# Kernel tuning notes

Hardware: AMD Instinct MI355X
Metric: run time of the kernel (lower is better)

Reference implementation:

```python
import jax, jax.numpy as jnp
import numpy as np

NUM_HEADS = 16
BN_EPS = 1e-5


def setup_inputs() -> dict:
    key = jax.random.key(0)
    ks = jax.random.split(key, 12)
    B, S, D = 8, 1024, 1024
    s = 1.0 / np.sqrt(D)
    return {
        "key": jax.random.normal(ks[0], (B, S, D), jnp.float32),
        "value": jax.random.normal(ks[1], (B, S, D), jnp.float32),
        "query": jax.random.normal(ks[2], (B, S, D), jnp.float32),
        "Wk": jax.random.normal(ks[3], (D, D), jnp.float32) * s,
        "bk": jax.random.normal(ks[4], (D,), jnp.float32) * s,
        "Wv": jax.random.normal(ks[5], (D, D), jnp.float32) * s,
        "bv": jax.random.normal(ks[6], (D,), jnp.float32) * s,
        "Wq": jax.random.normal(ks[7], (D, D), jnp.float32) * s,
        "bq": jax.random.normal(ks[8], (D,), jnp.float32) * s,
        "Wf": jax.random.normal(ks[9], (D, D), jnp.float32) * s,
        "bf": jax.random.normal(ks[10], (D,), jnp.float32) * s,
        "gamma": jnp.ones((D,), jnp.float32),
        "beta": jnp.zeros((D,), jnp.float32),
    }


def _mha(key, value, query, Wk, bk, Wv, bv, Wq, bq, Wf, bf, gamma, beta):
    B, S, D = query.shape
    H = NUM_HEADS
    d = D // H
    residual = query

    k = key @ Wk + bk      # [B, S, D]
    v = value @ Wv + bv
    q = query @ Wq + bq

    # Faithful to torch: raw row-major view(B*H, -1, d) — NOT the standard head transpose.
    k = k.reshape(B * H, -1, d)   # [B*H, S, d]
    v = v.reshape(B * H, -1, d)
    q = q.reshape(B * H, -1, d)

    # Faithful quirky scale: (dim_per_head // num_heads) ** -0.5
    scale = jnp.float32((d // H) ** (-0.5))

    scores = jnp.einsum('bqd,bkd->bqk', q, k) * scale          # [B*H, S, S]
    attention = jax.nn.softmax(scores, axis=2)
    context = jnp.einsum('bqk,bkd->bqd', attention, v)          # [B*H, S, d]

    context = context.reshape(B, -1, D)                         # [B, S, D]
    out = context @ Wf + bf

    # BatchNorm1d over channel dim D (training mode: batch stats over B and S, biased var)
    x = residual + out                                          # [B, S, D]
    mean = jnp.mean(x, axis=(0, 1))
    var = jnp.mean((x - mean) ** 2, axis=(0, 1))
    out = (x - mean) * jax.lax.rsqrt(var + BN_EPS) * gamma + beta
    return out, attention


def reference(key, value, query, Wk, bk, Wv, bv, Wq, bq, Wf, bf, gamma, beta):
    return _mha(key, value, query, Wk, bk, Wv, bv, Wq, bq, Wf, bf, gamma, beta)
```

## Files before the change

### kernel.cpp

```cpp
#include <hip/hip_runtime.h>
#include <hip/hip_bf16.h>
#include <stdint.h>

typedef __attribute__((ext_vector_type(8))) short     short8;
typedef __attribute__((ext_vector_type(8))) _Float16  f16x8;
typedef __attribute__((ext_vector_type(4))) float     f32x4;
typedef __attribute__((ext_vector_type(4))) unsigned short ushort4_t;

__device__ inline unsigned short f2bf(float f) {
    unsigned u = __float_as_uint(f);
    u += 0x7fffu + ((u >> 16) & 1u);
    return (unsigned short)(u >> 16);
}
__device__ inline float bf2f(unsigned short h) {
    return __uint_as_float(((unsigned)h) << 16);
}
__device__ inline unsigned short f2h(float f) {
    _Float16 h = (_Float16)f;
    unsigned short r;
    __builtin_memcpy(&r, &h, 2);
    return r;
}

__device__ inline void gload16(const void* g, void* lds) {
    unsigned loff = (unsigned)(uintptr_t)lds;
    loff = __builtin_amdgcn_readfirstlane(loff);
    auto l = (__attribute__((address_space(3))) unsigned int*)(uintptr_t)loff;
    auto p = (const __attribute__((address_space(1))) unsigned int*)(uintptr_t)g;
    __builtin_amdgcn_global_load_lds(p, l, 16, 0, 0);
}

__global__ void cvt3_f32_2b(const float4* __restrict__ k, const float4* __restrict__ q,
                            const float4* __restrict__ v,
                            ushort4_t* __restrict__ k16, ushort4_t* __restrict__ q16,
                            ushort4_t* __restrict__ v16, int n4) {
    const int which = blockIdx.y;
    const float4* in  = which == 0 ? k   : which == 1 ? q   : v;
    ushort4_t*    out = which == 0 ? k16 : which == 1 ? q16 : v16;
    const bool tof16 = (which < 2);
    for (int i = blockIdx.x * blockDim.x + threadIdx.x; i < n4; i += gridDim.x * blockDim.x) {
        float4 vv = in[i];
        ushort4_t r;
        if (tof16) { r.x = f2h(vv.x);  r.y = f2h(vv.y);  r.z = f2h(vv.z);  r.w = f2h(vv.w); }
        else       { r.x = f2bf(vv.x); r.y = f2bf(vv.y); r.z = f2bf(vv.z); r.w = f2bf(vv.w); }
        out[i] = r;
    }
}

__global__ void transpose_cvt4(const float* __restrict__ Wk, const float* __restrict__ Wq,
                               const float* __restrict__ Wv, const float* __restrict__ Wf,
                               unsigned short* __restrict__ WkT, unsigned short* __restrict__ WqT,
                               unsigned short* __restrict__ WvT, unsigned short* __restrict__ WfT) {
    const int which = blockIdx.z;
    const float* W = which == 0 ? Wk : which == 1 ? Wq : which == 2 ? Wv : Wf;
    unsigned short* WT = which == 0 ? WkT : which == 1 ? WqT : which == 2 ? WvT : WfT;
    const bool tof16 = (which < 2);
    const int dim = 1024;

    __shared__ float t[32][33];
    const int bx = blockIdx.x * 32, by = blockIdx.y * 32;
    const int tx = threadIdx.x, ty = threadIdx.y;
#pragma unroll
    for (int i = 0; i < 4; ++i)
        t[ty + 8 * i][tx] = W[(size_t)(by + ty + 8 * i) * dim + bx + tx];
    __syncthreads();
#pragma unroll
    for (int i = 0; i < 4; ++i) {
        float v = t[tx][ty + 8 * i];
        WT[(size_t)(bx + ty + 8 * i) * dim + by + tx] = tof16 ? f2h(v) : f2bf(v);
    }
}

__global__ void transpose_v(const unsigned short* __restrict__ v, unsigned short* __restrict__ vT) {
    const int bh = blockIdx.z, d0 = blockIdx.x * 32, s0 = blockIdx.y * 32;
    __shared__ unsigned short t[32][33];
    const int tx = threadIdx.x, ty = threadIdx.y;
    const size_t base = (size_t)bh << 16;
#pragma unroll
    for (int i = 0; i < 4; ++i)
        t[ty + 8 * i][tx] = v[base + (size_t)(s0 + ty + 8 * i) * 64 + d0 + tx];
    __syncthreads();
#pragma unroll
    for (int i = 0; i < 4; ++i)
        vT[base + (size_t)(d0 + ty + 8 * i) * 1024 + s0 + tx] = t[tx][ty + 8 * i];
}

template<int F16IN, int EPI>
__global__ __launch_bounds__(256, 2) void gemm_bt(
    const unsigned short* __restrict__ A,
    const unsigned short* __restrict__ Bt,
    const float* __restrict__ bias,
    unsigned short* __restrict__ C2b,
    const float* __restrict__ resid,
    float* __restrict__ Cf,
    int M, int N, int K, int nbx)
{
    const int bid = blockIdx.x;
    const int cpx = gridDim.x >> 3;
    const int swz = (bid & 7) * cpx + (bid >> 3);
    const int bm = swz / nbx, bn = swz % nbx;
    const int m0 = bm * 128, n0 = bn * 128;

    const int tid = threadIdx.x;
    const int w = tid >> 6, l = tid & 63, g = l >> 4, c = l & 15;
    const int wr = w >> 1, wc = w & 1;

    __shared__ unsigned short As[2][8192];
    __shared__ unsigned short Bs[2][8192];

    f32x4 acc[4][4] = {};

    const int srow = tid >> 3, scol = (tid & 7) * 8;
    const unsigned short* ApS = A  + (size_t)(m0 + srow) * K + scol;
    const unsigned short* BpS = Bt + (size_t)(n0 + srow) * K + scol;

    const int NT = K >> 6;

#define STAGE_GEMM(bufi, koff)                                                \
    do {                                                                      \
        _Pragma("unroll")                                                     \
        for (int i = 0; i < 4; ++i) {                                         \
            gload16(ApS + (size_t)i * 32 * K + (koff), &As[bufi][(i * 256 + tid - l) * 8]); \
            gload16(BpS + (size_t)i * 32 * K + (koff), &Bs[bufi][(i * 256 + tid - l) * 8]); \
        }                                                                     \
    } while (0)

#define COMPUTE_GEMM(bufi)                                                         \
    do {                                                                           \
        _Pragma("unroll")                                                          \
        for (int kk = 0; kk < 2; ++kk) {                                           \
            if constexpr (F16IN) {                                                 \
                f16x8 a[4], b[4];                                                  \
                _Pragma("unroll")                                                  \
                for (int mt = 0; mt < 4; ++mt)                                     \
                    a[mt] = *(const f16x8*)&As[bufi][(wr * 64 + mt * 16 + c) * 64 + kk * 32 + g * 8]; \
                _Pragma("unroll")                                                  \
                for (int nt = 0; nt < 4; ++nt)                                     \
                    b[nt] = *(const f16x8*)&Bs[bufi][(wc * 64 + nt * 16 + c) * 64 + kk * 32 + g * 8]; \
                _Pragma("unroll")                                                  \
                for (int mt = 0; mt < 4; ++mt)                                     \
                    _Pragma("unroll")                                              \
                    for (int nt = 0; nt < 4; ++nt)                                 \
                        acc[mt][nt] = __builtin_amdgcn_mfma_f32_16x16x32_f16(a[mt], b[nt], acc[mt][nt], 0, 0, 0); \
            } else {                                                               \
                short8 a[4], b[4];                                                 \
                _Pragma("unroll")                                                  \
                for (int mt = 0; mt < 4; ++mt)                                     \
                    a[mt] = *(const short8*)&As[bufi][(wr * 64 + mt * 16 + c) * 64 + kk * 32 + g * 8]; \
                _Pragma("unroll")                                                  \
                for (int nt = 0; nt < 4; ++nt)                                     \
                    b[nt] = *(const short8*)&Bs[bufi][(wc * 64 + nt * 16 + c) * 64 + kk * 32 + g * 8]; \
                _Pragma("unroll")                                                  \
                for (int mt = 0; mt < 4; ++mt)                                     \
                    _Pragma("unroll")                                              \
                    for (int nt = 0; nt < 4; ++nt)                                 \
                        acc[mt][nt] = __builtin_amdgcn_mfma_f32_16x16x32_bf16(a[mt], b[nt], acc[mt][nt], 0, 0, 0); \
            }                                                                      \
        }                                                                          \
    } while (0)

    STAGE_GEMM(0, 0);

#pragma unroll 2
    for (int kt = 0; kt < NT - 1; ++kt) {
        const int cur = kt & 1;
        STAGE_GEMM(cur ^ 1, (kt + 1) * 64);
        asm volatile("s_waitcnt vmcnt(8)" ::: "memory");
        __builtin_amdgcn_s_barrier();
        __builtin_amdgcn_sched_barrier(0);
        COMPUTE_GEMM(cur);
        __builtin_amdgcn_sched_barrier(0);
        __builtin_amdgcn_s_barrier();
    }
    asm volatile("s_waitcnt vmcnt(0)" ::: "memory");
    __builtin_amdgcn_s_barrier();
    __builtin_amdgcn_sched_barrier(0);
    COMPUTE_GEMM((NT - 1) & 1);

#undef STAGE_GEMM
#undef COMPUTE_GEMM

#pragma unroll
    for (int nt = 0; nt < 4; ++nt) {
        const int col = n0 + wc * 64 + nt * 16 + c;
        const float bs = bias[col];
#pragma unroll
        for (int mt = 0; mt < 4; ++mt) {
            const int row0 = m0 + wr * 64 + mt * 16 + g * 4;
#pragma unroll
            for (int r = 0; r < 4; ++r) {
                const float x = acc[mt][nt][r] + bs;
                const size_t idx = (size_t)(row0 + r) * N + col;
                if constexpr (EPI == 0) {
                    C2b[idx] = F16IN ? f2h(x) : f2bf(x);
                } else {
                    Cf[idx] = x + resid[idx];
                }
            }
        }
    }
}

__global__ __launch_bounds__(256, 4) void attn_kernel(
    const unsigned short* __restrict__ qf,
    const unsigned short* __restrict__ kf,
    const unsigned short* __restrict__ vT,
    float* __restrict__ attn_out,
    unsigned short* __restrict__ ctx)
{
    const int L = blockIdx.x;
    const int rb = (L >> 3) & 63;
    const int bh = ((L & 7) << 4) | (L >> 9);

    const int tid = threadIdx.x;
    const int w = tid >> 6, l = tid & 63, g = l >> 4, c = l & 15;
    const int n0 = w * 256;

    __shared__ unsigned short P[16 * 1024];
    __shared__ float rs_lds[4][16];
    __shared__ float inv_lds[16];

    const unsigned short* qb = qf + ((size_t)bh << 16) + (size_t)(rb * 16 + c) * 64 + g * 8;
    const f16x8 q0 = *(const f16x8*)(qb);
    const f16x8 q1 = *(const f16x8*)(qb + 32);

    const unsigned short* kb = kf + ((size_t)bh << 16);
    const unsigned swzc = ((unsigned)(c & 7)) << 4;
    const unsigned prow = (unsigned)c * 2048;

    ushort4_t pks[16];
    float rsum = 0.f;

#pragma unroll
    for (int t = 0; t < 16; ++t) {
        const unsigned short* kp = kb + (size_t)(n0 + t * 16 + c) * 64 + g * 8;
        const f16x8 a0 = *(const f16x8*)(kp);
        const f16x8 a1 = *(const f16x8*)(kp + 32);
        f32x4 s = {0.f, 0.f, 0.f, 0.f};
        s = __builtin_amdgcn_mfma_f32_16x16x32_f16(a0, q0, s, 0, 0, 0);
        s = __builtin_amdgcn_mfma_f32_16x16x32_f16(a1, q1, s, 0, 0, 0);

        const float p0 = __expf(s[0] * 0.5f);
        const float p1 = __expf(s[1] * 0.5f);
        const float p2 = __expf(s[2] * 0.5f);
        const float p3 = __expf(s[3] * 0.5f);
        rsum += (p0 + p1) + (p2 + p3);

        ushort4_t pk;
        pk.x = f2bf(p0); pk.y = f2bf(p1); pk.z = f2bf(p2); pk.w = f2bf(p3);
        pks[t] = pk;
        *(ushort4_t*)((char*)P + ((prow + (unsigned)(n0 * 2 + t * 32 + g * 8)) ^ swzc)) = pk;
    }

    rsum += __shfl_xor(rsum, 16);
    rsum += __shfl_xor(rsum, 32);
    if (g == 0) rs_lds[w][c] = rsum;
    __syncthreads();
    if (tid < 16)
        inv_lds[tid] = 1.0f / (rs_lds[0][tid] + rs_lds[1][tid] + rs_lds[2][tid] + rs_lds[3][tid]);
    __syncthreads();

    const int rA = l >> 3, jj = l & 7;
    const int rB = 8 + rA;
    const int slA = ((jj & 3) << 4) | rA;
    const int slB = ((jj & 3) << 4) | rB;
    const float invA = inv_lds[rA];
    const float invB = inv_lds[rB];
    float* aoA = attn_out + ((size_t)bh << 20) + (size_t)(rb * 16 + rA) * 1024 + n0;
    float* aoB = attn_out + ((size_t)bh << 20) + (size_t)(rb * 16 + rB) * 1024 + n0;

    f32x4 pacc = {0.f, 0.f, 0.f, 0.f};
    const unsigned short* vb = vT + ((size_t)bh << 16) + (size_t)(w * 16 + c) * 1024;
#pragma unroll
    for (int ks = 0; ks < 32; ++ks) {
        const short8 a = *(const short8*)((char*)P + ((prow + (unsigned)(ks * 64 + g * 16)) ^ swzc));
        const short8 b = *(const short8*)(vb + ks * 32 + g * 8);
        pacc = __builtin_amdgcn_mfma_f32_16x16x32_bf16(a, b, pacc, 0, 0, 0);
        if (ks & 1) {
            const int p = ks >> 2;
            const int t0 = 2 * p, t1 = t0 + 1;
            const bool isA = ((ks & 3) == 1);
            const int sl = isA ? slA : slB;
            unsigned long long e0, e1;
            __builtin_memcpy(&e0, &pks[t0], 8);
            __builtin_memcpy(&e1, &pks[t1], 8);
            const unsigned long long ea = __shfl(e0, sl, 64);
            const unsigned long long eb = __shfl(e1, sl, 64);
            const unsigned long long sel = (jj < 4) ? ea : eb;
            const float inv2 = isA ? invA : invB;
            f32x4 o;
            o[0] = bf2f((unsigned short)(sel      )) * inv2;
            o[1] = bf2f((unsigned short)(sel >> 16)) * inv2;
            o[2] = bf2f((unsigned short)(sel >> 32)) * inv2;
            o[3] = bf2f((unsigned short)(sel >> 48)) * inv2;
            float* dst = (isA ? aoA : aoB) + p * 32 + jj * 4;
            __builtin_nontemporal_store(o, (f32x4*)dst);
        }
    }
    unsigned short* cb = ctx + ((size_t)bh << 16) + (size_t)(rb * 16) * 64 + w * 16 + c;
#pragma unroll
    for (int r = 0; r < 4; ++r) {
        const int row = g * 4 + r;
        cb[(size_t)row * 64] = f2bf(pacc[r] * inv_lds[row]);
    }
}

__global__ void bn_stats(const float* __restrict__ x, float* __restrict__ psum, float* __restrict__ psq) {
    const int col = blockIdx.y * 256 + threadIdx.x;
    const int r0 = blockIdx.x * 128;
    float s = 0.f, q = 0.f;
#pragma unroll 4
    for (int r = 0; r < 128; ++r) {
        const float v = x[(size_t)(r0 + r) * 1024 + col];
        s += v; q += v * v;
    }
    psum[blockIdx.x * 1024 + col] = s;
    psq [blockIdx.x * 1024 + col] = q;
}

__global__ void bn_final(const float* __restrict__ psum, const float* __restrict__ psq,
                         const float* __restrict__ gamma, const float* __restrict__ beta,
                         float* __restrict__ ab) {
    const int cidx = threadIdx.x;
    float s = 0.f, q = 0.f;
#pragma unroll 8
    for (int i = 0; i < 64; ++i) { s += psum[i * 1024 + cidx]; q += psq[i * 1024 + cidx]; }
    const float mean = s * (1.0f / 8192.0f);
    const float var  = q * (1.0f / 8192.0f) - mean * mean;
    const float a = gamma[cidx] * rsqrtf(var + 1e-5f);
    ab[cidx]        = a;
    ab[1024 + cidx] = beta[cidx] - mean * a;
}

__global__ void bn_apply(const float4* __restrict__ x4, const float* __restrict__ ab, float4* __restrict__ o4) {
    const int n4 = 2 * 1024 * 1024;
    for (int i = blockIdx.x * blockDim.x + threadIdx.x; i < n4; i += gridDim.x * blockDim.x) {
        const float4 v = x4[i];
        const int c0 = (i & 255) << 2;
        float4 r;
        r.x = v.x * ab[c0 + 0] + ab[1024 + c0 + 0];
        r.y = v.y * ab[c0 + 1] + ab[1024 + c0 + 1];
        r.z = v.z * ab[c0 + 2] + ab[1024 + c0 + 2];
        r.w = v.w * ab[c0 + 3] + ab[1024 + c0 + 3];
        o4[i] = r;
    }
}

extern "C" void kernel_launch(void* const* d_in, const int* in_sizes, int n_in,
                              void* d_out, int out_size, void* d_ws, size_t ws_size,
                              hipStream_t stream) {
    (void)in_sizes; (void)n_in; (void)out_size; (void)ws_size;

    const float* key   = (const float*)d_in[0];
    const float* value = (const float*)d_in[1];
    const float* query = (const float*)d_in[2];
    const float* Wk = (const float*)d_in[3];
    const float* bk = (const float*)d_in[4];
    const float* Wv = (const float*)d_in[5];
    const float* bv = (const float*)d_in[6];
    const float* Wq = (const float*)d_in[7];
    const float* bq = (const float*)d_in[8];
    const float* Wf = (const float*)d_in[9];
    const float* bff = (const float*)d_in[10];
    const float* gamma = (const float*)d_in[11];
    const float* beta  = (const float*)d_in[12];

    char* ws = (char*)d_ws;
    const size_t MB = 1u << 20;
    unsigned short* key16   = (unsigned short*)(ws + 0);
    unsigned short* ctx     = (unsigned short*)(ws + 0);
    unsigned short* query16 = (unsigned short*)(ws + 16 * MB);
    unsigned short* value16 = (unsigned short*)(ws + 32 * MB);
    float*          xbuf    = (float*)(ws + 16 * MB);
    unsigned short* WkT = (unsigned short*)(ws + 48 * MB);
    unsigned short* WqT = (unsigned short*)(ws + 50 * MB);
    unsigned short* WvT = (unsigned short*)(ws + 52 * MB);
    unsigned short* WfT = (unsigned short*)(ws + 54 * MB);
    unsigned short* kbuf = (unsigned short*)(ws + 56 * MB);
    unsigned short* qbuf = (unsigned short*)(ws + 72 * MB);
    unsigned short* vbuf = (unsigned short*)(ws + 88 * MB);
    float* psum = (float*)(ws + 88 * MB);
    float* psq  = (float*)(ws + 88 * MB + 256 * 1024);
    float* ab   = (float*)(ws + 88 * MB + 512 * 1024);
    unsigned short* vTbuf = (unsigned short*)(ws + 104 * MB);

    float* out0 = (float*)d_out;
    float* attn = out0 + 8388608;

    const int n4big = 2 * 1024 * 1024;

    cvt3_f32_2b<<<dim3(1024, 3), 256, 0, stream>>>(
        (const float4*)key, (const float4*)query, (const float4*)value,
        (ushort4_t*)key16, (ushort4_t*)query16, (ushort4_t*)value16, n4big);

    dim3 tb(32, 8);
    transpose_cvt4<<<dim3(32, 32, 4), tb, 0, stream>>>(Wk, Wq, Wv, Wf, WkT, WqT, WvT, WfT);

    gemm_bt<1, 0><<<512, 256, 0, stream>>>(key16,   WkT, bk, kbuf, nullptr, nullptr, 8192, 1024, 1024, 8);
    gemm_bt<1, 0><<<512, 256, 0, stream>>>(query16, WqT, bq, qbuf, nullptr, nullptr, 8192, 1024, 1024, 8);
    gemm_bt<0, 0><<<512, 256, 0, stream>>>(value16, WvT, bv, vbuf, nullptr, nullptr, 8192, 1024, 1024, 8);

    transpose_v<<<dim3(2, 32, 128), tb, 0, stream>>>(vbuf, vTbuf);

    attn_kernel<<<8192, 256, 0, stream>>>(qbuf, kbuf, vTbuf, attn, ctx);

    gemm_bt<0, 1><<<512, 256, 0, stream>>>(ctx, WfT, bff, nullptr, query, xbuf, 8192, 1024, 1024, 8);

    bn_stats<<<dim3(64, 4), 256, 0, stream>>>(xbuf, psum, psq);
    bn_final<<<1, 1024, 0, stream>>>(psum, psq, gamma, beta, ab);
    bn_apply<<<2048, 256, 0, stream>>>((const float4*)xbuf, ab, (float4*)out0);
}
```

Before: 426.0 us.

## Batch QKV projections into one launch and fuse BN statistics into output GEMM

```diff
diff --git a/kernel.cpp b/kernel.cpp
--- a/kernel.cpp
+++ b/kernel.cpp
@@ -85,16 +85,23 @@
         vT[base + (size_t)(d0 + ty + 8 * i) * 1024 + s0 + tx] = t[tx][ty + 8 * i];
 }
 
-template<int F16IN, int EPI>
-__global__ __launch_bounds__(256, 2) void gemm_bt(
-    const unsigned short* __restrict__ A,
-    const unsigned short* __restrict__ Bt,
-    const float* __restrict__ bias,
-    unsigned short* __restrict__ C2b,
-    const float* __restrict__ resid,
-    float* __restrict__ Cf,
-    int M, int N, int K, int nbx)
+__global__ __launch_bounds__(256, 2) void qkv_gemm(
+    const unsigned short* __restrict__ k16, const unsigned short* __restrict__ q16,
+    const unsigned short* __restrict__ v16,
+    const unsigned short* __restrict__ WkT, const unsigned short* __restrict__ WqT,
+    const unsigned short* __restrict__ WvT,
+    const float* __restrict__ bk, const float* __restrict__ bq, const float* __restrict__ bv,
+    unsigned short* __restrict__ kout, unsigned short* __restrict__ qout,
+    unsigned short* __restrict__ vout)
 {
+    const int which = blockIdx.y;
+    const unsigned short* A   = which == 0 ? k16 : which == 1 ? q16 : v16;
+    const unsigned short* Bt  = which == 0 ? WkT : which == 1 ? WqT : WvT;
+    const float* bias         = which == 0 ? bk  : which == 1 ? bq  : bv;
+    unsigned short* C2b       = which == 0 ? kout : which == 1 ? qout : vout;
+    const bool f16in = (which < 2);
+    const int N = 1024, K = 1024, nbx = 8;
+
     const int bid = blockIdx.x;
     const int cpx = gridDim.x >> 3;
     const int swz = (bid & 7) * cpx + (bid >> 3);
@@ -129,7 +136,7 @@
     do {                                                                           \
         _Pragma("unroll")                                                          \
         for (int kk = 0; kk < 2; ++kk) {                                           \
-            if constexpr (F16IN) {                                                 \
+            if (f16in) {                                                           \
                 f16x8 a[4], b[4];                                                  \
                 _Pragma("unroll")                                                  \
                 for (int mt = 0; mt < 4; ++mt)                                     \
@@ -191,13 +198,134 @@
             for (int r = 0; r < 4; ++r) {
                 const float x = acc[mt][nt][r] + bs;
                 const size_t idx = (size_t)(row0 + r) * N + col;
-                if constexpr (EPI == 0) {
-                    C2b[idx] = F16IN ? f2h(x) : f2bf(x);
-                } else {
-                    Cf[idx] = x + resid[idx];
-                }
+                C2b[idx] = f16in ? f2h(x) : f2bf(x);
             }
         }
+    }
+}
+
+__global__ __launch_bounds__(256, 2) void gemm_out(
+    const unsigned short* __restrict__ A,
+    const unsigned short* __restrict__ Bt,
+    const float* __restrict__ bias,
+    const float* __restrict__ resid,
+    float* __restrict__ Cf,
+    float* __restrict__ psum,
+    float* __restrict__ psq)
+{
+    const int N = 1024, K = 1024, nbx = 8;
+    const int bid = blockIdx.x;
+    const int cpx = gridDim.x >> 3;
+    const int swz = (bid & 7) * cpx + (bid >> 3);
+    const int bm = swz / nbx, bn = swz % nbx;
+    const int m0 = bm * 128, n0 = bn * 128;
+
+    const int tid = threadIdx.x;
+    const int w = tid >> 6, l = tid & 63, g = l >> 4, c = l & 15;
+    const int wr = w >> 1, wc = w & 1;
+
+    __shared__ unsigned short As[2][8192];
+    __shared__ unsigned short Bs[2][8192];
+    __shared__ float sred[2][2][4][16][2];
+
+    f32x4 acc[4][4] = {};
+
+    const int srow = tid >> 3, scol = (tid & 7) * 8;
+    const unsigned short* ApS = A  + (size_t)(m0 + srow) * K + scol;
+    const unsigned short* BpS = Bt + (size_t)(n0 + srow) * K + scol;
+
+    const int NT = K >> 6;
+
+#define STAGE_GEMM(bufi, koff)                                                \
+    do {                                                                      \
+        _Pragma("unroll")                                                     \
+        for (int i = 0; i < 4; ++i) {                                         \
+            gload16(ApS + (size_t)i * 32 * K + (koff), &As[bufi][(i * 256 + tid - l) * 8]); \
+            gload16(BpS + (size_t)i * 32 * K + (koff), &Bs[bufi][(i * 256 + tid - l) * 8]); \
+        }                                                                     \
+    } while (0)
+
+#define COMPUTE_GEMM(bufi)                                                         \
+    do {                                                                           \
+        _Pragma("unroll")                                                          \
+        for (int kk = 0; kk < 2; ++kk) {                                           \
+            short8 a[4], b[4];                                                     \
+            _Pragma("unroll")                                                      \
+            for (int mt = 0; mt < 4; ++mt)                                         \
+                a[mt] = *(const short8*)&As[bufi][(wr * 64 + mt * 16 + c) * 64 + kk * 32 + g * 8]; \
+            _Pragma("unroll")                                                      \
+            for (int nt = 0; nt < 4; ++nt)                                         \
+                b[nt] = *(const short8*)&Bs[bufi][(wc * 64 + nt * 16 + c) * 64 + kk * 32 + g * 8]; \
+            _Pragma("unroll")                                                      \
+            for (int mt = 0; mt < 4; ++mt)                                         \
+                _Pragma("unroll")                                                  \
+                for (int nt = 0; nt < 4; ++nt)                                     \
+                    acc[mt][nt] = __builtin_amdgcn_mfma_f32_16x16x32_bf16(a[mt], b[nt], acc[mt][nt], 0, 0, 0); \
+        }                                                                          \
+    } while (0)
+
+    STAGE_GEMM(0, 0);
+
+#pragma unroll 2
+    for (int kt = 0; kt < NT - 1; ++kt) {
+        const int cur = kt & 1;
+        STAGE_GEMM(cur ^ 1, (kt + 1) * 64);
+        asm volatile("s_waitcnt vmcnt(8)" ::: "memory");
+        __builtin_amdgcn_s_barrier();
+        __builtin_amdgcn_sched_barrier(0);
+        COMPUTE_GEMM(cur);
+        __builtin_amdgcn_sched_barrier(0);
+        __builtin_amdgcn_s_barrier();
+    }
+    asm volatile("s_waitcnt vmcnt(0)" ::: "memory");
+    __builtin_amdgcn_s_barrier();
+    __builtin_amdgcn_sched_barrier(0);
+    COMPUTE_GEMM((NT - 1) & 1);
+
+#undef STAGE_GEMM
+#undef COMPUTE_GEMM
+
+    float s_nt[4] = {0.f, 0.f, 0.f, 0.f};
+    float q_nt[4] = {0.f, 0.f, 0.f, 0.f};
+#pragma unroll
+    for (int nt = 0; nt < 4; ++nt) {
+        const int col = n0 + wc * 64 + nt * 16 + c;
+        const float bs = bias[col];
+#pragma unroll
+        for (int mt = 0; mt < 4; ++mt) {
+            const int row0 = m0 + wr * 64 + mt * 16 + g * 4;
+#pragma unroll
+            for (int r = 0; r < 4; ++r) {
+                const size_t idx = (size_t)(row0 + r) * N + col;
+                const float xv = acc[mt][nt][r] + bs + resid[idx];
+                Cf[idx] = xv;
+                s_nt[nt] += xv;
+                q_nt[nt] += xv * xv;
+            }
+        }
+    }
+#pragma unroll
+    for (int nt = 0; nt < 4; ++nt) {
+        s_nt[nt] += __shfl_xor(s_nt[nt], 16);
+        s_nt[nt] += __shfl_xor(s_nt[nt], 32);
+        q_nt[nt] += __shfl_xor(q_nt[nt], 16);
+        q_nt[nt] += __shfl_xor(q_nt[nt], 32);
+    }
+    if (g == 0) {
+#pragma unroll
+        for (int nt = 0; nt < 4; ++nt) {
+            sred[wr][wc][nt][c][0] = s_nt[nt];
+            sred[wr][wc][nt][c][1] = q_nt[nt];
+        }
+    }
+    __syncthreads();
+    if (tid < 128) {
+        const int wc2 = tid >> 6, nt2 = (tid >> 4) & 3, c2 = tid & 15;
+        const float ss = sred[0][wc2][nt2][c2][0] + sred[1][wc2][nt2][c2][0];
+        const float qq = sred[0][wc2][nt2][c2][1] + sred[1][wc2][nt2][c2][1];
+        const int col = n0 + wc2 * 64 + nt2 * 16 + c2;
+        psum[bm * 1024 + col] = ss;
+        psq [bm * 1024 + col] = qq;
     }
 }
 
@@ -305,19 +433,6 @@
     }
 }
 
-__global__ void bn_stats(const float* __restrict__ x, float* __restrict__ psum, float* __restrict__ psq) {
-    const int col = blockIdx.y * 256 + threadIdx.x;
-    const int r0 = blockIdx.x * 128;
-    float s = 0.f, q = 0.f;
-#pragma unroll 4
-    for (int r = 0; r < 128; ++r) {
-        const float v = x[(size_t)(r0 + r) * 1024 + col];
-        s += v; q += v * v;
-    }
-    psum[blockIdx.x * 1024 + col] = s;
-    psq [blockIdx.x * 1024 + col] = q;
-}
-
 __global__ void bn_final(const float* __restrict__ psum, const float* __restrict__ psq,
                          const float* __restrict__ gamma, const float* __restrict__ beta,
                          float* __restrict__ ab) {
@@ -396,17 +511,15 @@
     dim3 tb(32, 8);
     transpose_cvt4<<<dim3(32, 32, 4), tb, 0, stream>>>(Wk, Wq, Wv, Wf, WkT, WqT, WvT, WfT);
 
-    gemm_bt<1, 0><<<512, 256, 0, stream>>>(key16,   WkT, bk, kbuf, nullptr, nullptr, 8192, 1024, 1024, 8);
-    gemm_bt<1, 0><<<512, 256, 0, stream>>>(query16, WqT, bq, qbuf, nullptr, nullptr, 8192, 1024, 1024, 8);
-    gemm_bt<0, 0><<<512, 256, 0, stream>>>(value16, WvT, bv, vbuf, nullptr, nullptr, 8192, 1024, 1024, 8);
+    qkv_gemm<<<dim3(512, 3), 256, 0, stream>>>(
+        key16, query16, value16, WkT, WqT, WvT, bk, bq, bv, kbuf, qbuf, vbuf);
 
     transpose_v<<<dim3(2, 32, 128), tb, 0, stream>>>(vbuf, vTbuf);
 
     attn_kernel<<<8192, 256, 0, stream>>>(qbuf, kbuf, vTbuf, attn, ctx);
 
-    gemm_bt<0, 1><<<512, 256, 0, stream>>>(ctx, WfT, bff, nullptr, query, xbuf, 8192, 1024, 1024, 8);
-
-    bn_stats<<<dim3(64, 4), 256, 0, stream>>>(xbuf, psum, psq);
+    gemm_out<<<512, 256, 0, stream>>>(ctx, WfT, bff, query, xbuf, psum, psq);
+
     bn_final<<<1, 1024, 0, stream>>>(psum, psq, gamma, beta, ab);
     bn_apply<<<2048, 256, 0, stream>>>((const float4*)xbuf, ab, (float4*)out0);
 }
```

After: 403.3 us (median of 2 runs). 5.3% less time.
